# Kernel optimization log

Hardware: AMD Instinct MI355X
Metric: run time of the kernel (lower is better)

Reference implementation:

```python
import jax, jax.numpy as jnp
import numpy as np

DIM = 256
NEG_SLOPE = 0.01  # torch F.leaky_relu default


def setup_inputs() -> dict:
    key = jax.random.key(0)
    ks = jax.random.split(key, 10)
    B, O, I, D = 16, 64, 512, DIM
    q = jax.random.normal(ks[0], (B, O, D), dtype=jnp.float32)
    k = jax.random.normal(ks[1], (B, I, D), dtype=jnp.float32)
    v = jax.random.normal(ks[2], (B, I, D), dtype=jnp.float32)
    mask = jax.random.randint(ks[3], (B, I), 0, 2).astype(bool)  # 1/True = pad
    s = 1.0 / np.sqrt(2 * D)
    # score MLP: Linear(2D -> D), tanh, Linear(D -> 1)
    W1 = jax.random.normal(ks[4], (D, 2 * D), dtype=jnp.float32) * s
    b1 = jnp.zeros((D,), dtype=jnp.float32)
    W2 = jax.random.normal(ks[5], (1, D), dtype=jnp.float32) * (1.0 / np.sqrt(D))
    b2 = jnp.zeros((1,), dtype=jnp.float32)
    # output projection fw: Linear(D -> D)
    Wf = jax.random.normal(ks[6], (D, D), dtype=jnp.float32) * (1.0 / np.sqrt(D))
    bf = jnp.zeros((D,), dtype=jnp.float32)
    return {"q": q, "k": k, "v": v, "mask": mask,
            "W1": W1, "b1": b1, "W2": W2, "b2": b2, "Wf": Wf, "bf": bf}


def reference(q, k, v, mask, W1, b1, W2, b2, Wf, bf):
    # Linear over concat([q, k]) decomposes exactly: W1 @ [q;k] = W1q@q + W1k@k
    D = q.shape[-1]
    W1q, W1k = W1[:, :D], W1[:, D:]
    qp = jnp.einsum('bod,hd->boh', q, W1q)          # (B, O, D)
    kp = jnp.einsum('bid,hd->bih', k, W1k)          # (B, I, D)
    h = jnp.tanh(qp[:, :, None, :] + kp[:, None, :, :] + b1)  # (B, O, I, D)
    score = jnp.einsum('boih,h->boi', h, W2[0]) + b2[0]       # (B, O, I)
    score = jnp.where(mask[:, None, :], -jnp.inf, score)
    attn = jax.nn.softmax(score, axis=-1)           # (B, O, I)
    out = jnp.einsum('boi,bid->bod', attn, v)       # (B, O, D)
    out = out @ Wf.T + bf                           # dropout in eval mode = identity
    out = jnp.where(out >= 0, out, NEG_SLOPE * out) # leaky_relu
    return out, attn
```

## Files before the change

kernel.cpp:

```cpp
#include <hip/hip_runtime.h>
#include <math.h>

#define DIM 256
#define BATCH 16
#define NO 64
#define NI 512
#define NEG_SLOPE 0.01f
#define CSCALE 2.885390081777927f
#define OT 2

__global__ __launch_bounds__(512) void mask_scan_kernel(
    const int* __restrict__ mask, int* __restrict__ idx,
    int* __restrict__ posArr, int* __restrict__ cnt)
{
  __shared__ int wtot[8];
  __shared__ int woff[8];
  const int b = blockIdx.x, t = threadIdx.x;
  const int lane = t & 63, wid = t >> 6;
  const int unm = (mask[b * NI + t] == 0) ? 1 : 0;
  unsigned long long bal = __ballot(unm);
  int my  = __popcll(bal & ((1ull << lane) - 1ull));
  if (lane == 0) wtot[wid] = __popcll(bal);
  __syncthreads();
  if (t == 0) {
    int acc = 0;
    for (int w = 0; w < 8; ++w) { woff[w] = acc; acc += wtot[w]; }
    cnt[b] = acc;
  }
  __syncthreads();
  int pos = woff[wid] + my;
  if (unm) idx[b * NI + pos] = t;
  posArr[b * NI + t] = unm ? pos : -1;
}

__global__ __launch_bounds__(256, 4) void proj_kernel(
    const float* __restrict__ q, const float* __restrict__ k,
    const float* __restrict__ W1, const float* __restrict__ b1,
    const float* __restrict__ Wf, const int* __restrict__ posArr,
    float* __restrict__ Eq, float* __restrict__ Ek4, float* __restrict__ WfT)
{
  __shared__ float smem[8704];

  const int t  = threadIdx.x;
  const int bx = blockIdx.x;

  if (bx >= 576) {
    const int tt = bx - 576;
    const int tr = tt >> 2, tc = tt & 3;
#pragma unroll
    for (int p = 0; p < 4; ++p) {
      int idx2 = p * 256 + t;
      int row = idx2 >> 4, j = idx2 & 15;
      float4 vv = *(const float4*)(Wf + (size_t)(tr * 64 + row) * 256 + tc * 64 + j * 4);
      *(float4*)&smem[row * 68 + j * 4] = vv;
    }
    __syncthreads();
#pragma unroll
    for (int p = 0; p < 4; ++p) {
      int idx2 = p * 256 + t;
      int row = idx2 >> 4, j = idx2 & 15;
      float4 ov;
      ov.x = smem[(j * 4 + 0) * 68 + row];
      ov.y = smem[(j * 4 + 1) * 68 + row];
      ov.z = smem[(j * 4 + 2) * 68 + row];
      ov.w = smem[(j * 4 + 3) * 68 + row];
      *(float4*)(WfT + (size_t)(tc * 64 + row) * 256 + tr * 64 + j * 4) = ov;
    }
    return;
  }

  float* At = smem;
  float* Wt = smem + 4352;

  const int tx = t & 15;
  const int ty = t >> 4;
  const int mt = bx >> 2;
  const int nt = bx & 3;
  const int r0 = mt * 64;
  const int h0 = nt * 64;
  const bool isq = (r0 < BATCH * NO);
  const float* src = isq ? (q + (size_t)r0 * DIM)
                         : (k + (size_t)(r0 - BATCH * NO) * DIM);
  const int coff = isq ? 0 : DIM;

  float acc[4][4] = {};

  for (int c0 = 0; c0 < DIM; c0 += 64) {
    __syncthreads();
#pragma unroll
    for (int p = 0; p < 4; ++p) {
      int idx2 = p * 256 + t;
      int row = idx2 >> 4, j = idx2 & 15;
      float4 av = *(const float4*)(src + (size_t)row * DIM + c0 + j * 4);
      At[(4 * j + 0) * 68 + row] = av.x;
      At[(4 * j + 1) * 68 + row] = av.y;
      At[(4 * j + 2) * 68 + row] = av.z;
      At[(4 * j + 3) * 68 + row] = av.w;
      float4 wv = *(const float4*)(W1 + (size_t)(h0 + row) * (2 * DIM) + coff + c0 + j * 4);
      Wt[(4 * j + 0) * 68 + row] = wv.x;
      Wt[(4 * j + 1) * 68 + row] = wv.y;
      Wt[(4 * j + 2) * 68 + row] = wv.z;
      Wt[(4 * j + 3) * 68 + row] = wv.w;
    }
    __syncthreads();
#pragma unroll
    for (int dk = 0; dk < 64; ++dk) {
      float4 a4 = *(const float4*)&At[dk * 68 + ty * 4];
      float4 w4 = *(const float4*)&Wt[dk * 68 + tx * 4];
      const float ar[4] = {a4.x, a4.y, a4.z, a4.w};
      const float wr[4] = {w4.x, w4.y, w4.z, w4.w};
#pragma unroll
      for (int rr = 0; rr < 4; ++rr)
#pragma unroll
        for (int cc = 0; cc < 4; ++cc)
          acc[rr][cc] = fmaf(ar[rr], wr[cc], acc[rr][cc]);
    }
  }

  if (isq) {
    float4 bv = *(const float4*)(b1 + h0 + tx * 4);
    const float br[4] = {bv.x, bv.y, bv.z, bv.w};
#pragma unroll
    for (int rr = 0; rr < 4; ++rr) {
      int r = r0 + ty * 4 + rr;
      float4 ov;
      ov.x = __builtin_amdgcn_exp2f((acc[rr][0] + br[0]) * CSCALE);
      ov.y = __builtin_amdgcn_exp2f((acc[rr][1] + br[1]) * CSCALE);
      ov.z = __builtin_amdgcn_exp2f((acc[rr][2] + br[2]) * CSCALE);
      ov.w = __builtin_amdgcn_exp2f((acc[rr][3] + br[3]) * CSCALE);
      *(float4*)(Eq + (size_t)r * DIM + h0 + tx * 4) = ov;
    }
  } else {
    int ig0 = r0 - BATCH * NO;
    int b   = ig0 >> 9;
    int i0  = (ig0 & 511) + ty * 4;
    int hq0 = (h0 >> 2) + tx;
#pragma unroll
    for (int rr = 0; rr < 4; ++rr) {
      int pos = posArr[b * NI + i0 + rr];
      if (pos >= 0) {
        float4 ov;
        ov.x = __builtin_amdgcn_exp2f(acc[rr][0] * CSCALE);
        ov.y = __builtin_amdgcn_exp2f(acc[rr][1] * CSCALE);
        ov.z = __builtin_amdgcn_exp2f(acc[rr][2] * CSCALE);
        ov.w = __builtin_amdgcn_exp2f(acc[rr][3] * CSCALE);
        *(float4*)(Ek4 + ((size_t)(b * 64 + hq0) * NI + pos) * 4) = ov;
      }
    }
  }
}

__device__ __forceinline__ void f4arr(float4 v, float* a) {
  a[0] = v.x; a[1] = v.y; a[2] = v.z; a[3] = v.w;
}

__global__ __launch_bounds__(512, 4) void attn_kernel(
    const float* __restrict__ Eq, const float* __restrict__ Ek4,
    const float* __restrict__ v, const int* __restrict__ idx,
    const int* __restrict__ posArr, const int* __restrict__ cnt,
    const float* __restrict__ W2, const float* __restrict__ b2,
    const float* __restrict__ WfT, const float* __restrict__ bf,
    float* __restrict__ out, float* __restrict__ attn_out)
{
  __shared__ float sc[OT][NI];
  __shared__ int   idxs[NI];
  __shared__ float pvp[8][OT][DIM];
  __shared__ float o0[OT][DIM];
  __shared__ float red4[8][OT];
  __shared__ float redw[8];

  const int t    = threadIdx.x;
  const int lane = t & 63;
  const int wid  = t >> 6;

  const int blk  = blockIdx.x;
  const int tile = (blk & 7) * 64 + (blk >> 3);
  const int b    = tile >> 5;
  const int bo0  = b * 64 + (tile & 31) * OT;

  const int cntb = cnt[b];
  idxs[t] = idx[b * NI + t];
  const int myPos = posArr[b * NI + t];

  float partial = (t < DIM) ? W2[t] : 0.f;
#pragma unroll
  for (int off = 32; off >= 1; off >>= 1) partial += __shfl_xor(partial, off, 64);
  if (lane == 0) redw[wid] = partial;
  __syncthreads();
  float sumw2 = 0.f;
#pragma unroll
  for (int w = 0; w < 8; ++w) sumw2 += redw[w];
  const float base = sumw2 + b2[0];

  const int j = t;
  const bool active = (j < cntb);
  const int jc = active ? j : (cntb > 0 ? cntb - 1 : 0);
  const float4* kb4 = (const float4*)Ek4 + (size_t)b * 64 * NI;
  const float* qrow0 = Eq + (size_t)(bo0 + 0) * DIM;
  const float* qrow1 = Eq + (size_t)(bo0 + 1) * DIM;

  float acc0 = 0.f, acc1 = 0.f;
  if (wid * 64 < cntb) {
#pragma unroll 8
    for (int hq = 0; hq < 64; ++hq) {
      float4 kq = kb4[(size_t)hq * NI + jc];
      float wr[4], q0r[4], q1r[4], kv[4];
      f4arr(*(const float4*)(W2 + hq * 4), wr);
      f4arr(*(const float4*)(qrow0 + hq * 4), q0r);
      f4arr(*(const float4*)(qrow1 + hq * 4), q1r);
      f4arr(kq, kv);
#pragma unroll
      for (int pr = 0; pr < 2; ++pr) {
        const int ea = pr * 2, eb = pr * 2 + 1;
        float A0 = fmaf(q0r[ea], kv[ea], 1.f);
        float B0 = fmaf(q0r[eb], kv[eb], 1.f);
        float N0 = fmaf(wr[eb], A0, wr[ea] * B0);
        acc0 = fmaf(N0, __builtin_amdgcn_rcpf(A0 * B0), acc0);
        float A1 = fmaf(q1r[ea], kv[ea], 1.f);
        float B1 = fmaf(q1r[eb], kv[eb], 1.f);
        float N1 = fmaf(wr[eb], A1, wr[ea] * B1);
        acc1 = fmaf(N1, __builtin_amdgcn_rcpf(A1 * B1), acc1);
      }
    }
  }

  float s0 = active ? (base - 2.f * acc0) : -INFINITY;
  float s1 = active ? (base - 2.f * acc1) : -INFINITY;

  float p0 = __builtin_amdgcn_exp2f(s0 * 1.4426950408889634f);
  float p1 = __builtin_amdgcn_exp2f(s1 * 1.4426950408889634f);
  float ps0 = p0, ps1 = p1;
#pragma unroll
  for (int off = 32; off >= 1; off >>= 1) {
    ps0 += __shfl_xor(ps0, off, 64);
    ps1 += __shfl_xor(ps1, off, 64);
  }
  __syncthreads();
  if (lane == 0) { red4[wid][0] = ps0; red4[wid][1] = ps1; }
  __syncthreads();
  float ss0 = 0.f, ss1 = 0.f;
#pragma unroll
  for (int w = 0; w < 8; ++w) { ss0 += red4[w][0]; ss1 += red4[w][1]; }
  const float a0 = p0 * __builtin_amdgcn_rcpf(ss0);
  const float a1 = p1 * __builtin_amdgcn_rcpf(ss1);
  sc[0][j] = a0;
  sc[1][j] = a1;
  __syncthreads();

  {
    float w0 = (myPos >= 0) ? sc[0][myPos] : 0.f;
    float w1 = (myPos >= 0) ? sc[1][myPos] : 0.f;
    attn_out[(size_t)(bo0 + 0) * NI + t] = w0;
    attn_out[(size_t)(bo0 + 1) * NI + t] = w1;
  }

  {
    const int d4 = lane;
    float4 av0 = {0.f, 0.f, 0.f, 0.f};
    float4 av1 = {0.f, 0.f, 0.f, 0.f};
    const float4* vb4 = (const float4*)(v + (size_t)b * NI * DIM);
    const int jend = min(wid * 64 + 64, cntb);
#pragma unroll 4
    for (int jb = wid * 64; jb < jend; ++jb) {
      int row = idxs[jb];
      float sa0 = sc[0][jb], sa1 = sc[1][jb];
      float4 vv = vb4[(size_t)row * 64 + d4];
      av0.x = fmaf(sa0, vv.x, av0.x);
      av0.y = fmaf(sa0, vv.y, av0.y);
      av0.z = fmaf(sa0, vv.z, av0.z);
      av0.w = fmaf(sa0, vv.w, av0.w);
      av1.x = fmaf(sa1, vv.x, av1.x);
      av1.y = fmaf(sa1, vv.y, av1.y);
      av1.z = fmaf(sa1, vv.z, av1.z);
      av1.w = fmaf(sa1, vv.w, av1.w);
    }
    *(float4*)&pvp[wid][0][d4 * 4] = av0;
    *(float4*)&pvp[wid][1][d4 * 4] = av1;
  }
  __syncthreads();
  {
    int oo = t >> 8, d = t & 255;
    float sacc = 0.f;
#pragma unroll
    for (int w = 0; w < 8; ++w) sacc += pvp[w][oo][d];
    o0[oo][d] = sacc;
  }
  __syncthreads();

  if (t < DIM) {
    const int d = t;
    float f0 = 0.f, f1 = 0.f;
#pragma unroll 8
    for (int e4 = 0; e4 < 64; ++e4) {
      float oa[4], ob[4];
      f4arr(*(const float4*)&o0[0][e4 * 4], oa);
      f4arr(*(const float4*)&o0[1][e4 * 4], ob);
#pragma unroll
      for (int c = 0; c < 4; ++c) {
        float wv = WfT[(size_t)(e4 * 4 + c) * DIM + d];
        f0 = fmaf(oa[c], wv, f0);
        f1 = fmaf(ob[c], wv, f1);
      }
    }
    float bfv = bf[d];
    f0 += bfv; f1 += bfv;
    f0 = (f0 >= 0.f) ? f0 : NEG_SLOPE * f0;
    f1 = (f1 >= 0.f) ? f1 : NEG_SLOPE * f1;
    out[(size_t)(bo0 + 0) * DIM + d] = f0;
    out[(size_t)(bo0 + 1) * DIM + d] = f1;
  }
}

extern "C" void kernel_launch(void* const* d_in, const int* in_sizes, int n_in,
                              void* d_out, int out_size, void* d_ws, size_t ws_size,
                              hipStream_t stream) {
  const float* q    = (const float*)d_in[0];
  const float* k    = (const float*)d_in[1];
  const float* v    = (const float*)d_in[2];
  const int*   mask = (const int*)d_in[3];
  const float* W1   = (const float*)d_in[4];
  const float* b1   = (const float*)d_in[5];
  const float* W2   = (const float*)d_in[6];
  const float* b2   = (const float*)d_in[7];
  const float* Wf   = (const float*)d_in[8];
  const float* bf   = (const float*)d_in[9];

  float* out      = (float*)d_out;
  float* attn_out = out + (size_t)BATCH * NO * DIM;

  float* Eq   = (float*)d_ws;
  float* Ek4  = Eq + (size_t)BATCH * NO * DIM;
  float* WfT  = Ek4 + (size_t)BATCH * DIM * NI;
  int*   idx  = (int*)(WfT + (size_t)DIM * DIM);
  int*   pos  = idx + BATCH * NI;
  int*   cnt  = pos + BATCH * NI;

  mask_scan_kernel<<<BATCH, 512, 0, stream>>>(mask, idx, pos, cnt);
  proj_kernel<<<592, 256, 0, stream>>>(q, k, W1, b1, Wf, pos, Eq, Ek4, WfT);
  attn_kernel<<<(BATCH * NO) / OT, 512, 0, stream>>>(Eq, Ek4, v, idx, pos, cnt,
                                                     W2, b2, WfT, bf, out, attn_out);
}
```

Measured before the change: 140.3 us.

## Use split-bf16 MFMA for projection GEMM with register-prefetched tiles

Replaces the scalar FMA 64x64 projection tile in proj_kernel with bf16 MFMA 16x16x32 instructions. Each fp32 value is split into a high and low bf16 pair, and three MFMAs (hi*hi, hi*lo, lo*hi) keep precision close to fp32. Global loads for the next K chunk are issued into registers before the current chunk's MFMAs, so load latency overlaps compute. The cost is extra conversion ALU work, a larger LDS footprint, and scattered scalar stores in the epilogue. proj_kernel is only part of the total time, and the attention kernel probably dominates.

```diff
diff --git a/kernel.cpp b/kernel.cpp
--- a/kernel.cpp
+++ b/kernel.cpp
@@ -8,6 +8,10 @@
 #define NEG_SLOPE 0.01f
 #define CSCALE 2.885390081777927f
 #define OT 2
+
+typedef float f32x4 __attribute__((ext_vector_type(4)));
+typedef __bf16 bf16x8 __attribute__((ext_vector_type(8)));
+typedef unsigned int u32x4 __attribute__((ext_vector_type(4)));
 
 __global__ __launch_bounds__(512) void mask_scan_kernel(
     const int* __restrict__ mask, int* __restrict__ idx,
@@ -33,18 +37,37 @@
   posArr[b * NI + t] = unm ? pos : -1;
 }
 
+__device__ __forceinline__ void split2(float f, unsigned int& hi16, float& lo) {
+  unsigned int u = __builtin_bit_cast(unsigned int, f);
+  unsigned int h = (u + 0x7FFFu + ((u >> 16) & 1u)) & 0xFFFF0000u;
+  hi16 = h >> 16;
+  lo = f - __builtin_bit_cast(float, h);
+}
+__device__ __forceinline__ unsigned int rne16(float f) {
+  unsigned int u = __builtin_bit_cast(unsigned int, f);
+  return (u + 0x7FFFu + ((u >> 16) & 1u)) >> 16;
+}
+
+struct __align__(8) U2 { unsigned int x, y; };
+
+#define OFF_AH 0
+#define OFF_AL 9216
+#define OFF_WH 18432
+#define OFF_WL 27648
+
 __global__ __launch_bounds__(256, 4) void proj_kernel(
     const float* __restrict__ q, const float* __restrict__ k,
     const float* __restrict__ W1, const float* __restrict__ b1,
     const float* __restrict__ Wf, const int* __restrict__ posArr,
     float* __restrict__ Eq, float* __restrict__ Ek4, float* __restrict__ WfT)
 {
-  __shared__ float smem[8704];
+  __shared__ __align__(16) char smemRaw[36864];
 
   const int t  = threadIdx.x;
   const int bx = blockIdx.x;
 
   if (bx >= 576) {
+    float* smem = (float*)smemRaw;
     const int tt = bx - 576;
     const int tr = tt >> 2, tc = tt & 3;
 #pragma unroll
@@ -69,11 +92,6 @@
     return;
   }
 
-  float* At = smem;
-  float* Wt = smem + 4352;
-
-  const int tx = t & 15;
-  const int ty = t >> 4;
   const int mt = bx >> 2;
   const int nt = bx & 3;
   const int r0 = mt * 64;
@@ -83,70 +101,109 @@
                          : (k + (size_t)(r0 - BATCH * NO) * DIM);
   const int coff = isq ? 0 : DIM;
 
-  float acc[4][4] = {};
-
-  for (int c0 = 0; c0 < DIM; c0 += 64) {
+  const int srow = t >> 4;
+  const int sc4  = t & 15;
+
+  const int lane = t & 63, w = t >> 6;
+  const int m0w = (w >> 1) * 32, n0w = (w & 1) * 32;
+  const int lr = lane & 15, lg = lane >> 4;
+
+  f32x4 acc[2][2] = {};
+
+  float4 aR[4], wR[4];
+#define LOADC(c0_)                                                              \
+  _Pragma("unroll")                                                             \
+  for (int p = 0; p < 4; ++p) {                                                 \
+    int row = srow + p * 16;                                                    \
+    aR[p] = *(const float4*)(src + (size_t)row * DIM + (c0_) + sc4 * 4);        \
+    wR[p] = *(const float4*)(W1 + (size_t)(h0 + row) * (2 * DIM) + coff + (c0_) + sc4 * 4); \
+  }
+
+  LOADC(0)
+
+  for (int c = 0; c < 4; ++c) {
+#pragma unroll
+    for (int p = 0; p < 4; ++p) {
+      int row = srow + p * 16;
+      int boff = row * 144 + sc4 * 8;
+      unsigned int h0_, h1_, h2_, h3_;
+      float l0, l1, l2, l3;
+      split2(aR[p].x, h0_, l0); split2(aR[p].y, h1_, l1);
+      split2(aR[p].z, h2_, l2); split2(aR[p].w, h3_, l3);
+      *(U2*)(smemRaw + OFF_AH + boff) = { h0_ | (h1_ << 16), h2_ | (h3_ << 16) };
+      *(U2*)(smemRaw + OFF_AL + boff) = { rne16(l0) | (rne16(l1) << 16),
+                                          rne16(l2) | (rne16(l3) << 16) };
+      split2(wR[p].x, h0_, l0); split2(wR[p].y, h1_, l1);
+      split2(wR[p].z, h2_, l2); split2(wR[p].w, h3_, l3);
+      *(U2*)(smemRaw + OFF_WH + boff) = { h0_ | (h1_ << 16), h2_ | (h3_ << 16) };
+      *(U2*)(smemRaw + OFF_WL + boff) = { rne16(l0) | (rne16(l1) << 16),
+                                          rne16(l2) | (rne16(l3) << 16) };
+    }
     __syncthreads();
-#pragma unroll
-    for (int p = 0; p < 4; ++p) {
-      int idx2 = p * 256 + t;
-      int row = idx2 >> 4, j = idx2 & 15;
-      float4 av = *(const float4*)(src + (size_t)row * DIM + c0 + j * 4);
-      At[(4 * j + 0) * 68 + row] = av.x;
-      At[(4 * j + 1) * 68 + row] = av.y;
-      At[(4 * j + 2) * 68 + row] = av.z;
-      At[(4 * j + 3) * 68 + row] = av.w;
-      float4 wv = *(const float4*)(W1 + (size_t)(h0 + row) * (2 * DIM) + coff + c0 + j * 4);
-      Wt[(4 * j + 0) * 68 + row] = wv.x;
-      Wt[(4 * j + 1) * 68 + row] = wv.y;
-      Wt[(4 * j + 2) * 68 + row] = wv.z;
-      Wt[(4 * j + 3) * 68 + row] = wv.w;
+
+    if (c < 3) { LOADC((c + 1) * 64) }
+
+#pragma unroll
+    for (int kk = 0; kk < 2; ++kk) {
+      const int kb = kk * 64 + lg * 16;
+      bf16x8 ah[2], al[2], bh[2], bl[2];
+#pragma unroll
+      for (int mi = 0; mi < 2; ++mi) {
+        int row = m0w + mi * 16 + lr;
+        ah[mi] = __builtin_bit_cast(bf16x8, *(const u32x4*)(smemRaw + OFF_AH + row * 144 + kb));
+        al[mi] = __builtin_bit_cast(bf16x8, *(const u32x4*)(smemRaw + OFF_AL + row * 144 + kb));
+      }
+#pragma unroll
+      for (int ni = 0; ni < 2; ++ni) {
+        int row = n0w + ni * 16 + lr;
+        bh[ni] = __builtin_bit_cast(bf16x8, *(const u32x4*)(smemRaw + OFF_WH + row * 144 + kb));
+        bl[ni] = __builtin_bit_cast(bf16x8, *(const u32x4*)(smemRaw + OFF_WL + row * 144 + kb));
+      }
+#pragma unroll
+      for (int mi = 0; mi < 2; ++mi)
+#pragma unroll
+        for (int ni = 0; ni < 2; ++ni) {
+          acc[mi][ni] = __builtin_amdgcn_mfma_f32_16x16x32_bf16(ah[mi], bh[ni], acc[mi][ni], 0, 0, 0);
+          acc[mi][ni] = __builtin_amdgcn_mfma_f32_16x16x32_bf16(ah[mi], bl[ni], acc[mi][ni], 0, 0, 0);
+          acc[mi][ni] = __builtin_amdgcn_mfma_f32_16x16x32_bf16(al[mi], bh[ni], acc[mi][ni], 0, 0, 0);
+        }
     }
     __syncthreads();
-#pragma unroll
-    for (int dk = 0; dk < 64; ++dk) {
-      float4 a4 = *(const float4*)&At[dk * 68 + ty * 4];
-      float4 w4 = *(const float4*)&Wt[dk * 68 + tx * 4];
-      const float ar[4] = {a4.x, a4.y, a4.z, a4.w};
-      const float wr[4] = {w4.x, w4.y, w4.z, w4.w};
-#pragma unroll
-      for (int rr = 0; rr < 4; ++rr)
-#pragma unroll
-        for (int cc = 0; cc < 4; ++cc)
-          acc[rr][cc] = fmaf(ar[rr], wr[cc], acc[rr][cc]);
-    }
   }
 
   if (isq) {
-    float4 bv = *(const float4*)(b1 + h0 + tx * 4);
-    const float br[4] = {bv.x, bv.y, bv.z, bv.w};
-#pragma unroll
-    for (int rr = 0; rr < 4; ++rr) {
-      int r = r0 + ty * 4 + rr;
-      float4 ov;
-      ov.x = __builtin_amdgcn_exp2f((acc[rr][0] + br[0]) * CSCALE);
-      ov.y = __builtin_amdgcn_exp2f((acc[rr][1] + br[1]) * CSCALE);
-      ov.z = __builtin_amdgcn_exp2f((acc[rr][2] + br[2]) * CSCALE);
-      ov.w = __builtin_amdgcn_exp2f((acc[rr][3] + br[3]) * CSCALE);
-      *(float4*)(Eq + (size_t)r * DIM + h0 + tx * 4) = ov;
+#pragma unroll
+    for (int ni = 0; ni < 2; ++ni) {
+      int h = h0 + n0w + ni * 16 + lr;
+      float b1v = b1[h];
+#pragma unroll
+      for (int mi = 0; mi < 2; ++mi)
+#pragma unroll
+        for (int rg = 0; rg < 4; ++rg) {
+          int r = r0 + m0w + mi * 16 + lg * 4 + rg;
+          Eq[(size_t)r * DIM + h] =
+              __builtin_amdgcn_exp2f((acc[mi][ni][rg] + b1v) * CSCALE);
+        }
     }
   } else {
-    int ig0 = r0 - BATCH * NO;
-    int b   = ig0 >> 9;
-    int i0  = (ig0 & 511) + ty * 4;
-    int hq0 = (h0 >> 2) + tx;
-#pragma unroll
-    for (int rr = 0; rr < 4; ++rr) {
-      int pos = posArr[b * NI + i0 + rr];
-      if (pos >= 0) {
-        float4 ov;
-        ov.x = __builtin_amdgcn_exp2f(acc[rr][0] * CSCALE);
-        ov.y = __builtin_amdgcn_exp2f(acc[rr][1] * CSCALE);
-        ov.z = __builtin_amdgcn_exp2f(acc[rr][2] * CSCALE);
-        ov.w = __builtin_amdgcn_exp2f(acc[rr][3] * CSCALE);
-        *(float4*)(Ek4 + ((size_t)(b * 64 + hq0) * NI + pos) * 4) = ov;
-      }
-    }
+    const int rk0 = r0 - BATCH * NO;
+    const int b = rk0 >> 9;
+    const int ib = rk0 & 511;
+#pragma unroll
+    for (int mi = 0; mi < 2; ++mi)
+#pragma unroll
+      for (int rg = 0; rg < 4; ++rg) {
+        int i = ib + m0w + mi * 16 + lg * 4 + rg;
+        int pos = posArr[b * NI + i];
+        if (pos >= 0) {
+#pragma unroll
+          for (int ni = 0; ni < 2; ++ni) {
+            int h = h0 + n0w + ni * 16 + lr;
+            Ek4[((size_t)(b * 64 + (h >> 2)) * NI + pos) * 4 + (h & 3)] =
+                __builtin_amdgcn_exp2f(acc[mi][ni][rg] * CSCALE);
+          }
+        }
+      }
   }
 }
 
```

After: 124.2 us. -11.5%, faster.
